# Performance work log

Hardware: AMD Instinct MI355X
Metric: run time of the kernel (lower is better)

The kernel has to match this reference:

```python
import jax, jax.numpy as jnp
import numpy as np

B, S, D = 16, 2048, 128

def setup_inputs() -> dict:
    key = jax.random.key(0)
    kq, kk, kv = jax.random.split(key, 3)
    return {
        "query": jax.random.normal(kq, (B, S, D), dtype=jnp.float32),
        "key": jax.random.normal(kk, (B, S, D), dtype=jnp.float32),
        "value": jax.random.normal(kv, (B, S, D), dtype=jnp.float32),
    }

def reference(query, key, value):
    # query: (B, S2, d), key: (B, S1, d), value: (B, S1, d)
    d_k = query.shape[-1]
    scale = 1.0 / jnp.sqrt(jnp.asarray(d_k, dtype=query.dtype))
    # (B, S2, S1) attention scores
    att = jnp.einsum('bqd,bkd->bqk', query, key) * scale
    att = jax.nn.softmax(att, axis=-1)
    # (B, S2, d_v)
    return jnp.einsum('bqk,bkd->bqd', att, value)
```

## Files before the change

### kernel.cpp

```cpp
#include <hip/hip_runtime.h>

#define B_N 16
#define S_LEN 2048
#define D_DIM 128
#define TK 32
#define NTH 32
#define PSTR 40

typedef __attribute__((ext_vector_type(16))) float f32x16;
typedef __attribute__((ext_vector_type(8)))  short short8;
typedef const __attribute__((address_space(1))) void* gp1;
typedef __attribute__((address_space(3))) void* sp3;
#define GLL(g, l) __builtin_amdgcn_global_load_lds((gp1)(const void*)(g), (sp3)(void*)(l), 16, 0, 0)

static __device__ __forceinline__ unsigned short f2bf(float f) {
  unsigned u = __builtin_bit_cast(unsigned, f);
  return (unsigned short)((u + 0x7fffu + ((u >> 16) & 1u)) >> 16);
}

__global__ __launch_bounds__(256)
void prep_kernel(const float* __restrict__ K, const float* __restrict__ V,
                 unsigned short* __restrict__ Kb, unsigned short* __restrict__ VT) {
  __shared__ unsigned short lds[64 * 66];
  int bx = blockIdx.x;
  int t  = threadIdx.x;
  if (bx < 4096) {
    size_t i = ((size_t)bx * 256 + t) * 4;
    float4 v = *(const float4*)(K + i);
    unsigned lo = (unsigned)f2bf(v.x) | ((unsigned)f2bf(v.y) << 16);
    unsigned hi = (unsigned)f2bf(v.z) | ((unsigned)f2bf(v.w) << 16);
    *(uint2*)(Kb + i) = make_uint2(lo, hi);
  } else {
    int bi = bx - 4096;
    int b  = bi & 15;
    int st = (bi >> 4) & 31;
    int dt = bi >> 9;
    const float* Vb = V + ((size_t)b * S_LEN + st * 64) * D_DIM + dt * 64;
    unsigned short* VTb = VT + ((size_t)b * D_DIM + dt * 64) * S_LEN + st * 64;
#pragma unroll
    for (int rep = 0; rep < 4; ++rep) {
      int idx = rep * 256 + t;
      int i  = idx >> 4;
      int j4 = (idx & 15) * 4;
      float4 v = *(const float4*)(Vb + (size_t)i * D_DIM + j4);
      unsigned lo = (unsigned)f2bf(v.x) | ((unsigned)f2bf(v.y) << 16);
      unsigned hi = (unsigned)f2bf(v.z) | ((unsigned)f2bf(v.w) << 16);
      *(uint2*)&lds[i * 66 + j4] = make_uint2(lo, hi);
    }
    __syncthreads();
#pragma unroll
    for (int rep = 0; rep < 4; ++rep) {
      int idx = rep * 256 + t;
      int dd = idx >> 4;
      int s4 = (idx & 15) * 4;
      unsigned short e0 = lds[(s4 + 0) * 66 + dd];
      unsigned short e1 = lds[(s4 + 1) * 66 + dd];
      unsigned short e2 = lds[(s4 + 2) * 66 + dd];
      unsigned short e3 = lds[(s4 + 3) * 66 + dd];
      *(uint2*)(VTb + (size_t)dd * S_LEN + s4) =
          make_uint2((unsigned)e0 | ((unsigned)e1 << 16),
                     (unsigned)e2 | ((unsigned)e3 << 16));
    }
  }
}

__global__ __launch_bounds__(512, 2)
void attn_kernel(const float* __restrict__ Q, const unsigned short* __restrict__ Kb,
                 const unsigned short* __restrict__ VT, float* __restrict__ O) {
  __shared__ __align__(16) char smem[86016];

  const int tid  = threadIdx.x;
  const int wave = tid >> 6;
  const int g    = wave >> 2;
  const int w4   = wave & 3;
  const int lane = tid & 63;
  const int l32  = lane & 31;
  const int half = lane >> 5;

  const int i     = blockIdx.x;
  const int b     = (i & 7) * 2 + ((i >> 3) & 1);
  const int qtile = i >> 4;
  const int qbase = qtile * 128 + w4 * 32;

  const float* Qb = Q + (size_t)b * S_LEN * D_DIM;
  const unsigned short* Kbb = Kb + (size_t)b * S_LEN * D_DIM;
  const unsigned short* VTb = VT + (size_t)b * D_DIM * S_LEN;

  unsigned short* kb0 = (unsigned short*)smem + (size_t)g * 2 * 4096;
  unsigned short* vb0 = (unsigned short*)(smem + 32768) + (size_t)g * 2 * 4096;
  unsigned short* pw  = (unsigned short*)(smem + 65536) + wave * 32 * PSTR;

  {
    const int T0 = g * NTH;
#pragma unroll
    for (int cc = 0; cc < 2; ++cc) {
      int c = w4 * 2 + cc;
      int rl = 4 * c + (lane >> 4);
      int lbk = (lane & 15) ^ (rl & 15);
      GLL(Kbb + (size_t)(T0 * TK + rl) * D_DIM + lbk * 8, kb0 + c * 512);
      int dv = 16 * c + (lane >> 2);
      int lbv = (lane & 3) ^ ((dv >> 1) & 3);
      GLL(VTb + (size_t)dv * S_LEN + T0 * TK + lbv * 8, vb0 + c * 512);
    }
  }

  short8 qa[8];
  {
    const float* qp = Qb + (size_t)(qbase + l32) * D_DIM + half * 8;
#pragma unroll
    for (int ks = 0; ks < 8; ++ks) {
      float4 a0 = *(const float4*)(qp + ks * 16);
      float4 a1 = *(const float4*)(qp + ks * 16 + 4);
      short8 f;
      f[0] = (short)f2bf(a0.x); f[1] = (short)f2bf(a0.y);
      f[2] = (short)f2bf(a0.z); f[3] = (short)f2bf(a0.w);
      f[4] = (short)f2bf(a1.x); f[5] = (short)f2bf(a1.y);
      f[6] = (short)f2bf(a1.z); f[7] = (short)f2bf(a1.w);
      qa[ks] = f;
    }
  }

  const f32x16 zf16 = {0.f,0.f,0.f,0.f,0.f,0.f,0.f,0.f,0.f,0.f,0.f,0.f,0.f,0.f,0.f,0.f};
  f32x16 oacc[4];
  float lsum[16];
#pragma unroll
  for (int dt = 0; dt < 4; ++dt) oacc[dt] = zf16;
#pragma unroll
  for (int r = 0; r < 16; ++r) lsum[r] = 0.f;

  const float SC = 0.08838834764831845f * 1.4426950408889634f;

  for (int t = 0; t < NTH; ++t) {
    __syncthreads();
    const int cb = t & 1;
    const unsigned short* kbc = kb0 + cb * 4096;
    const unsigned short* vbc = vb0 + cb * 4096;

    if (t + 1 < NTH) {
      const int nb = cb ^ 1;
      const int T = g * NTH + t + 1;
#pragma unroll
      for (int cc = 0; cc < 2; ++cc) {
        int c = w4 * 2 + cc;
        int rl = 4 * c + (lane >> 4);
        int lbk = (lane & 15) ^ (rl & 15);
        GLL(Kbb + (size_t)(T * TK + rl) * D_DIM + lbk * 8, kb0 + nb * 4096 + c * 512);
        int dv = 16 * c + (lane >> 2);
        int lbv = (lane & 3) ^ ((dv >> 1) & 3);
        GLL(VTb + (size_t)dv * S_LEN + T * TK + lbv * 8, vb0 + nb * 4096 + c * 512);
      }
    }

    f32x16 sacc = zf16;
#pragma unroll
    for (int ks = 0; ks < 8; ++ks) {
      int pk = (ks * 2 + half) ^ (l32 & 15);
      short8 kf = *(const short8*)&kbc[l32 * D_DIM + pk * 8];
      sacc = __builtin_amdgcn_mfma_f32_32x32x16_bf16(qa[ks], kf, sacc, 0, 0, 0);
    }

#pragma unroll
    for (int reg = 0; reg < 16; ++reg) {
      float p = exp2f(sacc[reg] * SC);
      lsum[reg] += p;
      int row = (reg & 3) + 8 * (reg >> 2) + 4 * half;
      pw[row * PSTR + l32] = f2bf(p);
    }

    short8 pf[2];
#pragma unroll
    for (int ks2 = 0; ks2 < 2; ++ks2)
      pf[ks2] = *(const short8*)&pw[l32 * PSTR + ks2 * 16 + half * 8];

#pragma unroll
    for (int ks2 = 0; ks2 < 2; ++ks2) {
#pragma unroll
      for (int dt = 0; dt < 4; ++dt) {
        int dv = dt * 32 + l32;
        int pv = (ks2 * 2 + half) ^ ((dv >> 1) & 3);
        short8 vf = *(const short8*)&vbc[dv * TK + pv * 8];
        oacc[dt] = __builtin_amdgcn_mfma_f32_32x32x16_bf16(pf[ks2], vf, oacc[dt], 0, 0, 0);
      }
    }
  }

#pragma unroll
  for (int reg = 0; reg < 16; ++reg) {
    float s = lsum[reg];
    s += __shfl_xor(s, 1);
    s += __shfl_xor(s, 2);
    s += __shfl_xor(s, 4);
    s += __shfl_xor(s, 8);
    s += __shfl_xor(s, 16);
    lsum[reg] = s;
  }

  __syncthreads();
  float* mo = (float*)(smem + w4 * 16512);
  float* ml = (float*)(smem + w4 * 16512 + 16384);
  if (g == 1) {
#pragma unroll
    for (int reg = 0; reg < 16; ++reg) {
      int row = (reg & 3) + 8 * (reg >> 2) + 4 * half;
#pragma unroll
      for (int dt = 0; dt < 4; ++dt)
        mo[row * 128 + dt * 32 + l32] = oacc[dt][reg];
      if (l32 == 0) ml[row] = lsum[reg];
    }
  }
  __syncthreads();
  if (g == 0) {
    float* Ob = O + (size_t)b * S_LEN * D_DIM;
#pragma unroll
    for (int reg = 0; reg < 16; ++reg) {
      int row = (reg & 3) + 8 * (reg >> 2) + 4 * half;
      float linv = 1.f / (lsum[reg] + ml[row]);
#pragma unroll
      for (int dt = 0; dt < 4; ++dt)
        Ob[(size_t)(qbase + row) * D_DIM + dt * 32 + l32] =
            (oacc[dt][reg] + mo[row * 128 + dt * 32 + l32]) * linv;
    }
  }
}

extern "C" void kernel_launch(void* const* d_in, const int* in_sizes, int n_in,
                              void* d_out, int out_size, void* d_ws, size_t ws_size,
                              hipStream_t stream) {
  const float* Q = (const float*)d_in[0];
  const float* K = (const float*)d_in[1];
  const float* V = (const float*)d_in[2];
  float* O = (float*)d_out;
  unsigned short* Kb = (unsigned short*)d_ws;
  unsigned short* VT = Kb + (size_t)B_N * S_LEN * D_DIM;
  prep_kernel<<<dim3(4096 + 1024), dim3(256), 0, stream>>>(K, V, Kb, VT);
  attn_kernel<<<dim3(256), dim3(512), 0, stream>>>(Q, Kb, VT, O);
}
```

Baseline: 146.5 us.

## Compute transposed scores to keep P in registers, drop LDS P staging

Swaps the MFMA operand order so the score tile comes out transposed. Each lane then holds probabilities laid out so the PV MFMA A-operand can be built with a few cross-half shuffles instead of a write/read round trip through a per-wave LDS buffer. This shrinks LDS use and lets the row-sum become a per-lane accumulation with one final shuffle. It also folds the softmax scale into Q before conversion, uses a packed bf16 conversion builtin, and precomputes the LDS and global offsets outside the loop. The risks are more register pressure and bf16 rounding of the pre-scaled Q.

```diff
diff --git a/kernel.cpp b/kernel.cpp
--- a/kernel.cpp
+++ b/kernel.cpp
@@ -1,11 +1,11 @@
 #include <hip/hip_runtime.h>
+#include <hip/hip_bf16.h>
 
 #define B_N 16
 #define S_LEN 2048
 #define D_DIM 128
 #define TK 32
 #define NTH 32
-#define PSTR 40
 
 typedef __attribute__((ext_vector_type(16))) float f32x16;
 typedef __attribute__((ext_vector_type(8)))  short short8;
@@ -16,6 +16,16 @@
 static __device__ __forceinline__ unsigned short f2bf(float f) {
   unsigned u = __builtin_bit_cast(unsigned, f);
   return (unsigned short)((u + 0x7fffu + ((u >> 16) & 1u)) >> 16);
+}
+
+static __device__ __forceinline__ unsigned pk_bf16(float a, float b) {
+#if __has_builtin(__builtin_amdgcn_cvt_pk_bf16_f32)
+  typedef __attribute__((ext_vector_type(2))) __bf16 bf16x2;
+  bf16x2 r = __builtin_amdgcn_cvt_pk_bf16_f32(a, b);
+  return __builtin_bit_cast(unsigned, r);
+#else
+  return (unsigned)f2bf(a) | ((unsigned)f2bf(b) << 16);
+#endif
 }
 
 __global__ __launch_bounds__(256)
@@ -27,9 +37,7 @@
   if (bx < 4096) {
     size_t i = ((size_t)bx * 256 + t) * 4;
     float4 v = *(const float4*)(K + i);
-    unsigned lo = (unsigned)f2bf(v.x) | ((unsigned)f2bf(v.y) << 16);
-    unsigned hi = (unsigned)f2bf(v.z) | ((unsigned)f2bf(v.w) << 16);
-    *(uint2*)(Kb + i) = make_uint2(lo, hi);
+    *(uint2*)(Kb + i) = make_uint2(pk_bf16(v.x, v.y), pk_bf16(v.z, v.w));
   } else {
     int bi = bx - 4096;
     int b  = bi & 15;
@@ -43,9 +51,7 @@
       int i  = idx >> 4;
       int j4 = (idx & 15) * 4;
       float4 v = *(const float4*)(Vb + (size_t)i * D_DIM + j4);
-      unsigned lo = (unsigned)f2bf(v.x) | ((unsigned)f2bf(v.y) << 16);
-      unsigned hi = (unsigned)f2bf(v.z) | ((unsigned)f2bf(v.w) << 16);
-      *(uint2*)&lds[i * 66 + j4] = make_uint2(lo, hi);
+      *(uint2*)&lds[i * 66 + j4] = make_uint2(pk_bf16(v.x, v.y), pk_bf16(v.z, v.w));
     }
     __syncthreads();
 #pragma unroll
@@ -67,7 +73,7 @@
 __global__ __launch_bounds__(512, 2)
 void attn_kernel(const float* __restrict__ Q, const unsigned short* __restrict__ Kb,
                  const unsigned short* __restrict__ VT, float* __restrict__ O) {
-  __shared__ __align__(16) char smem[86016];
+  __shared__ __align__(16) char smem[66048];
 
   const int tid  = threadIdx.x;
   const int wave = tid >> 6;
@@ -86,24 +92,42 @@
   const unsigned short* Kbb = Kb + (size_t)b * S_LEN * D_DIM;
   const unsigned short* VTb = VT + (size_t)b * D_DIM * S_LEN;
 
-  unsigned short* kb0 = (unsigned short*)smem + (size_t)g * 2 * 4096;
-  unsigned short* vb0 = (unsigned short*)(smem + 32768) + (size_t)g * 2 * 4096;
-  unsigned short* pw  = (unsigned short*)(smem + 65536) + wave * 32 * PSTR;
-
-  {
-    const int T0 = g * NTH;
-#pragma unroll
-    for (int cc = 0; cc < 2; ++cc) {
-      int c = w4 * 2 + cc;
-      int rl = 4 * c + (lane >> 4);
-      int lbk = (lane & 15) ^ (rl & 15);
-      GLL(Kbb + (size_t)(T0 * TK + rl) * D_DIM + lbk * 8, kb0 + c * 512);
-      int dv = 16 * c + (lane >> 2);
-      int lbv = (lane & 3) ^ ((dv >> 1) & 3);
-      GLL(VTb + (size_t)dv * S_LEN + T0 * TK + lbv * 8, vb0 + c * 512);
-    }
-  }
-
+  unsigned short* kb0 = (unsigned short*)smem + g * 8192;
+  unsigned short* vb0 = (unsigned short*)(smem + 32768) + g * 8192;
+
+  const unsigned short* kgp[2];
+  const unsigned short* vgp[2];
+  unsigned short* kdst[2][2];
+  unsigned short* vdst[2][2];
+#pragma unroll
+  for (int cc = 0; cc < 2; ++cc) {
+    int c  = w4 * 2 + cc;
+    int rl = 4 * c + (lane >> 4);
+    int lbk = (lane & 15) ^ (rl & 15);
+    kgp[cc] = Kbb + (size_t)(g * NTH * TK + rl) * D_DIM + lbk * 8;
+    int dv = 16 * c + (lane >> 2);
+    int lbv = (lane & 3) ^ ((dv >> 1) & 3);
+    vgp[cc] = VTb + (size_t)dv * S_LEN + g * NTH * TK + lbv * 8;
+    kdst[0][cc] = kb0 + c * 512;  kdst[1][cc] = kb0 + 4096 + c * 512;
+    vdst[0][cc] = vb0 + c * 512;  vdst[1][cc] = vb0 + 4096 + c * 512;
+  }
+#pragma unroll
+  for (int cc = 0; cc < 2; ++cc) { GLL(kgp[cc], kdst[0][cc]); GLL(vgp[cc], vdst[0][cc]); }
+
+  int kOff[8], vOff[8];
+#pragma unroll
+  for (int ks = 0; ks < 8; ++ks)
+    kOff[ks] = (l32 * D_DIM + (((ks << 1) + half) ^ (l32 & 15)) * 8) * 2;
+#pragma unroll
+  for (int ks2 = 0; ks2 < 2; ++ks2)
+#pragma unroll
+    for (int dt = 0; dt < 4; ++dt) {
+      int dv = dt * 32 + l32;
+      int pv = ((ks2 << 1) + half) ^ ((dv >> 1) & 3);
+      vOff[ks2 * 4 + dt] = (dv * TK + pv * 8) * 2;
+    }
+
+  const float SC = 0.08838834764831845f * 1.4426950408889634f;
   short8 qa[8];
   {
     const float* qp = Qb + (size_t)(qbase + l32) * D_DIM + half * 8;
@@ -111,89 +135,75 @@
     for (int ks = 0; ks < 8; ++ks) {
       float4 a0 = *(const float4*)(qp + ks * 16);
       float4 a1 = *(const float4*)(qp + ks * 16 + 4);
-      short8 f;
-      f[0] = (short)f2bf(a0.x); f[1] = (short)f2bf(a0.y);
-      f[2] = (short)f2bf(a0.z); f[3] = (short)f2bf(a0.w);
-      f[4] = (short)f2bf(a1.x); f[5] = (short)f2bf(a1.y);
-      f[6] = (short)f2bf(a1.z); f[7] = (short)f2bf(a1.w);
-      qa[ks] = f;
+      union { unsigned u[4]; short8 s; } pu;
+      pu.u[0] = pk_bf16(a0.x * SC, a0.y * SC);
+      pu.u[1] = pk_bf16(a0.z * SC, a0.w * SC);
+      pu.u[2] = pk_bf16(a1.x * SC, a1.y * SC);
+      pu.u[3] = pk_bf16(a1.z * SC, a1.w * SC);
+      qa[ks] = pu.s;
     }
   }
 
   const f32x16 zf16 = {0.f,0.f,0.f,0.f,0.f,0.f,0.f,0.f,0.f,0.f,0.f,0.f,0.f,0.f,0.f,0.f};
   f32x16 oacc[4];
-  float lsum[16];
 #pragma unroll
   for (int dt = 0; dt < 4; ++dt) oacc[dt] = zf16;
-#pragma unroll
-  for (int r = 0; r < 16; ++r) lsum[r] = 0.f;
-
-  const float SC = 0.08838834764831845f * 1.4426950408889634f;
+  float lp[4] = {0.f, 0.f, 0.f, 0.f};
 
   for (int t = 0; t < NTH; ++t) {
     __syncthreads();
     const int cb = t & 1;
-    const unsigned short* kbc = kb0 + cb * 4096;
-    const unsigned short* vbc = vb0 + cb * 4096;
+    const char* kbc = (const char*)kb0 + cb * 8192;
+    const char* vbc = (const char*)vb0 + cb * 8192;
 
     if (t + 1 < NTH) {
       const int nb = cb ^ 1;
-      const int T = g * NTH + t + 1;
 #pragma unroll
       for (int cc = 0; cc < 2; ++cc) {
-        int c = w4 * 2 + cc;
-        int rl = 4 * c + (lane >> 4);
-        int lbk = (lane & 15) ^ (rl & 15);
-        GLL(Kbb + (size_t)(T * TK + rl) * D_DIM + lbk * 8, kb0 + nb * 4096 + c * 512);
-        int dv = 16 * c + (lane >> 2);
-        int lbv = (lane & 3) ^ ((dv >> 1) & 3);
-        GLL(VTb + (size_t)dv * S_LEN + T * TK + lbv * 8, vb0 + nb * 4096 + c * 512);
+        kgp[cc] += TK * D_DIM;  GLL(kgp[cc], kdst[nb][cc]);
+        vgp[cc] += TK;          GLL(vgp[cc], vdst[nb][cc]);
       }
     }
 
     f32x16 sacc = zf16;
 #pragma unroll
     for (int ks = 0; ks < 8; ++ks) {
-      int pk = (ks * 2 + half) ^ (l32 & 15);
-      short8 kf = *(const short8*)&kbc[l32 * D_DIM + pk * 8];
-      sacc = __builtin_amdgcn_mfma_f32_32x32x16_bf16(qa[ks], kf, sacc, 0, 0, 0);
-    }
-
-#pragma unroll
-    for (int reg = 0; reg < 16; ++reg) {
-      float p = exp2f(sacc[reg] * SC);
-      lsum[reg] += p;
-      int row = (reg & 3) + 8 * (reg >> 2) + 4 * half;
-      pw[row * PSTR + l32] = f2bf(p);
-    }
-
-    short8 pf[2];
-#pragma unroll
-    for (int ks2 = 0; ks2 < 2; ++ks2)
-      pf[ks2] = *(const short8*)&pw[l32 * PSTR + ks2 * 16 + half * 8];
+      short8 kf = *(const short8*)(kbc + kOff[ks]);
+      sacc = __builtin_amdgcn_mfma_f32_32x32x16_bf16(kf, qa[ks], sacc, 0, 0, 0);
+    }
+
+    float p[16];
+#pragma unroll
+    for (int r = 0; r < 16; ++r) p[r] = exp2f(sacc[r]);
+#pragma unroll
+    for (int r = 0; r < 16; ++r) lp[r & 3] += p[r];
+    unsigned w[8];
+#pragma unroll
+    for (int j = 0; j < 8; ++j) w[j] = pk_bf16(p[2 * j], p[2 * j + 1]);
 
 #pragma unroll
     for (int ks2 = 0; ks2 < 2; ++ks2) {
+      const int a = ks2 * 4;
+      unsigned x0 = (unsigned)__shfl_xor((int)w[a + 0], 32);
+      unsigned x1 = (unsigned)__shfl_xor((int)w[a + 1], 32);
+      unsigned x2 = (unsigned)__shfl_xor((int)w[a + 2], 32);
+      unsigned x3 = (unsigned)__shfl_xor((int)w[a + 3], 32);
+      union { unsigned u[4]; short8 s; } pu;
+      pu.u[0] = half ? x2 : w[a + 0];
+      pu.u[1] = half ? x3 : w[a + 1];
+      pu.u[2] = half ? w[a + 2] : x0;
+      pu.u[3] = half ? w[a + 3] : x1;
+      short8 pf = pu.s;
 #pragma unroll
       for (int dt = 0; dt < 4; ++dt) {
-        int dv = dt * 32 + l32;
-        int pv = (ks2 * 2 + half) ^ ((dv >> 1) & 3);
-        short8 vf = *(const short8*)&vbc[dv * TK + pv * 8];
-        oacc[dt] = __builtin_amdgcn_mfma_f32_32x32x16_bf16(pf[ks2], vf, oacc[dt], 0, 0, 0);
+        short8 vf = *(const short8*)(vbc + vOff[ks2 * 4 + dt]);
+        oacc[dt] = __builtin_amdgcn_mfma_f32_32x32x16_bf16(pf, vf, oacc[dt], 0, 0, 0);
       }
     }
   }
 
-#pragma unroll
-  for (int reg = 0; reg < 16; ++reg) {
-    float s = lsum[reg];
-    s += __shfl_xor(s, 1);
-    s += __shfl_xor(s, 2);
-    s += __shfl_xor(s, 4);
-    s += __shfl_xor(s, 8);
-    s += __shfl_xor(s, 16);
-    lsum[reg] = s;
-  }
+  float lt = (lp[0] + lp[1]) + (lp[2] + lp[3]);
+  lt += __shfl_xor(lt, 32);
 
   __syncthreads();
   float* mo = (float*)(smem + w4 * 16512);
@@ -205,16 +215,17 @@
 #pragma unroll
       for (int dt = 0; dt < 4; ++dt)
         mo[row * 128 + dt * 32 + l32] = oacc[dt][reg];
-      if (l32 == 0) ml[row] = lsum[reg];
-    }
+    }
+    if (half == 0) ml[l32] = lt;
   }
   __syncthreads();
   if (g == 0) {
+    float tot = lt + ml[l32];
     float* Ob = O + (size_t)b * S_LEN * D_DIM;
 #pragma unroll
     for (int reg = 0; reg < 16; ++reg) {
       int row = (reg & 3) + 8 * (reg >> 2) + 4 * half;
-      float linv = 1.f / (lsum[reg] + ml[row]);
+      float linv = 1.f / __shfl(tot, row);
 #pragma unroll
       for (int dt = 0; dt < 4; ++dt)
         Ob[(size_t)(qbase + row) * D_DIM + dt * 32 + l32] =
```

Result: no change. 149.3 us (+1.9%).
